# Kernel optimization log

Measured on AMD Instinct MI355X. Metric: run time of the kernel, lower is better.

Reference implementation:

```python
import jax, jax.numpy as jnp
import numpy as np


def setup_inputs() -> dict:
    key = jax.random.key(0)
    k1, k2 = jax.random.split(key)
    B, N, M = 16, 4096, 4096
    xyz1 = jax.random.normal(k1, (B, N, 3), dtype=jnp.float32)
    xyz2 = jax.random.normal(k2, (B, M, 3), dtype=jnp.float32)
    return {"xyz1": xyz1, "xyz2": xyz2}


def reference(xyz1, xyz2):
    sq1 = jnp.sum(xyz1 * xyz1, axis=-1)            # [B, N]
    sq2 = jnp.sum(xyz2 * xyz2, axis=-1)            # [B, M]
    inner = jnp.einsum('bnd,bmd->bnm', xyz1, xyz2)  # [B, N, M]
    d = sq1[:, :, None] + sq2[:, None, :] - 2.0 * inner
    dist1 = jnp.min(d, axis=2)  # nearest in xyz2 for each point of xyz1, [B, N]
    dist2 = jnp.min(d, axis=1)  # nearest in xyz1 for each point of xyz2, [B, M]
    return (jnp.mean(dist1), jnp.mean(dist2))
```

## Files before the change

kernel.cpp:

```cpp
#include <hip/hip_runtime.h>
#include <float.h>

#define BATCH  16
#define NPTS   4096
#define TOTALP (BATCH * NPTS)
#define NQ     (2 * TOTALP)

typedef _Float16 half8  __attribute__((ext_vector_type(8)));
typedef float    f32x16 __attribute__((ext_vector_type(16)));

#define ONE2 0x3C003C00u

__device__ __forceinline__ unsigned enc(float f)
{
    unsigned b = __float_as_uint(f);
    return (b & 0x80000000u) ? ~b : (b | 0x80000000u);
}
__device__ __forceinline__ float dec(unsigned k)
{
    return (k & 0x80000000u) ? __uint_as_float(k & 0x7FFFFFFFu)
                             : __uint_as_float(~k);
}

__device__ __forceinline__ unsigned pk(_Float16 lo, _Float16 hi)
{
    const unsigned a = (unsigned)__builtin_bit_cast(unsigned short, lo);
    const unsigned b = (unsigned)__builtin_bit_cast(unsigned short, hi);
    return a | (b << 16);
}

__device__ __forceinline__ float min16(const f32x16& d, float acc)
{
    const float m1 = fminf(fminf(d[0],  d[1]),  d[2]);
    const float m2 = fminf(fminf(d[3],  d[4]),  d[5]);
    const float m3 = fminf(fminf(d[6],  d[7]),  d[8]);
    const float m4 = fminf(fminf(d[9],  d[10]), d[11]);
    const float m5 = fminf(fminf(d[12], d[13]), d[14]);
    const float m6 = fminf(fminf(m1, m2), m3);
    const float m7 = fminf(fminf(m4, m5), d[15]);
    return fminf(fminf(m6, m7), acc);
}

__global__ __launch_bounds__(256) void prep_kernel(
    const float* __restrict__ xyz1, const float* __restrict__ xyz2,
    uint4* __restrict__ packQ, uint4* __restrict__ planes,
    unsigned* __restrict__ keys, float* __restrict__ out)
{
    const int i = blockIdx.x * 256 + threadIdx.x;
    if (i == 0) { out[0] = 0.0f; out[1] = 0.0f; }
    keys[i] = 0xFFFFFFFFu;

    const float* src = (i < TOTALP) ? xyz1 : xyz2;
    const int p = i & (TOTALP - 1);
    const float x = src[3 * p + 0];
    const float y = src[3 * p + 1];
    const float z = src[3 * p + 2];
    const float sq = x * x + y * y + z * z;
    const _Float16 sh = (_Float16)sq;
    const _Float16 sl = (_Float16)(sq - (float)sh);

    const _Float16 vxh = (_Float16)x, vyh = (_Float16)y, vzh = (_Float16)z;
    const _Float16 vxl = (_Float16)(x - (float)vxh);
    const _Float16 vyl = (_Float16)(y - (float)vyh);
    const _Float16 vzl = (_Float16)(z - (float)vzh);
    planes[i]      = make_uint4(pk(vxh, vyh), pk(vzh, vxh),
                                pk(vyh, vzh), pk(vxl, vyl));
    planes[NQ + i] = make_uint4(pk(vzl, vxl), pk(vyl, vzl),
                                ONE2,         pk(sh, sl));

    const float ux = -2.0f * x, uy = -2.0f * y, uz = -2.0f * z;
    const _Float16 uxh = (_Float16)ux, uyh = (_Float16)uy, uzh = (_Float16)uz;
    const _Float16 uxl = (_Float16)(ux - (float)uxh);
    const _Float16 uyl = (_Float16)(uy - (float)uyh);
    const _Float16 uzl = (_Float16)(uz - (float)uzh);
    packQ[i] = make_uint4(pk(uxh, uyh), pk(uzh, uxl), pk(uyl, uzl), pk(sh, sl));
}

__global__ __launch_bounds__(256, 4) void chamfer_stream(
    const uint4* __restrict__ packQ, const uint4* __restrict__ planes,
    unsigned* __restrict__ keys)
{
    const int blk = blockIdx.x;
    const int ch  = blk & 7;
    const int qc  = (blk >> 3) & 7;
    const int b   = (blk >> 6) & 15;
    const int dir = blk >> 10;

    const int lane = threadIdx.x & 63;
    const int wv   = threadIdx.x >> 6;
    const int n32  = lane & 31;
    const int half = lane >> 5;

    const int qbase = dir * TOTALP + b * NPTS + qc * 512 + wv * 128;
    half8 bfrag[4];
#pragma unroll
    for (int qf = 0; qf < 4; ++qf) {
        const uint4 d = packQ[qbase + qf * 32 + n32];
        const uint4 u = half ? make_uint4(d.y, d.z, d.w, ONE2)
                             : make_uint4(d.x, d.y, d.z, d.x);
        bfrag[qf] = __builtin_bit_cast(half8, u);
    }

    float acc[4];
#pragma unroll
    for (int qf = 0; qf < 4; ++qf) acc[qf] = FLT_MAX;

    f32x16 cz;
#pragma unroll
    for (int r = 0; r < 16; ++r) cz[r] = 0.0f;

    const uint4* __restrict__ ap =
        planes + (size_t)half * NQ + (dir ^ 1) * TOTALP + b * NPTS + ch * 512;

    uint4 t0 = ap[0 * 32 + n32];
    uint4 t1 = ap[1 * 32 + n32];
    uint4 t2 = ap[2 * 32 + n32];
    uint4 t3 = ap[3 * 32 + n32];

    for (int t = 0; t < 16; ++t) {
        const uint4 tn = ap[(((t + 4) & 15) * 32) + n32];
        const half8 af = __builtin_bit_cast(half8, t0);
#pragma unroll
        for (int qf = 0; qf < 4; ++qf) {
            const f32x16 dd = __builtin_amdgcn_mfma_f32_32x32x16_f16(
                af, bfrag[qf], cz, 0, 0, 0);
            acc[qf] = min16(dd, acc[qf]);
        }
        t0 = t1; t1 = t2; t2 = t3; t3 = tn;
    }

#pragma unroll
    for (int qf = 0; qf < 4; ++qf) {
        float v = acc[qf];
        v = fminf(v, __shfl_xor(v, 32));
        if (lane < 32)
            atomicMin(&keys[qbase + qf * 32 + n32], enc(v));
    }
}

__global__ __launch_bounds__(256) void chamfer_final_atomic(
    const unsigned* __restrict__ keys, float* __restrict__ out)
{
    const int q0  = blockIdx.x * 512 + threadIdx.x;
    const int dir = q0 >> 16;

    float d = dec(keys[q0]) + dec(keys[q0 + 256]);

    for (int off = 32; off > 0; off >>= 1)
        d += __shfl_down(d, off);

    __shared__ float wsum[4];
    const int lane = threadIdx.x & 63;
    const int wv   = threadIdx.x >> 6;
    if (lane == 0) wsum[wv] = d;
    __syncthreads();
    if (threadIdx.x == 0) {
        float s = wsum[0] + wsum[1] + wsum[2] + wsum[3];
        atomicAdd(&out[dir], s * (1.0f / (float)TOTALP));
    }
}

__global__ void zero_out_kernel(float* __restrict__ out)
{
    if (threadIdx.x == 0) { out[0] = 0.0f; out[1] = 0.0f; }
}

__global__ __launch_bounds__(256) void chamfer_raw_kernel(
    const float* __restrict__ xyz1, const float* __restrict__ xyz2,
    float* __restrict__ out)
{
    const int blk = blockIdx.x;
    const int dir = blk >> 8;
    const int idx = blk & 255;
    const int b   = idx >> 4;
    const int n0  = (idx & 15) << 8;

    const float* __restrict__ own = (dir == 0 ? xyz1 : xyz2) + (size_t)b * NPTS * 3;
    const float* __restrict__ opp = (dir == 0 ? xyz2 : xyz1) + (size_t)b * NPTS * 3;

    const int n = n0 + threadIdx.x;
    const float ax = own[3 * n + 0];
    const float ay = own[3 * n + 1];
    const float az = own[3 * n + 2];

    float best = FLT_MAX;
    for (int m = 0; m < NPTS; m += 4) {
#pragma unroll
        for (int u = 0; u < 4; ++u) {
            const float px = opp[3 * (m + u) + 0];
            const float py = opp[3 * (m + u) + 1];
            const float pz = opp[3 * (m + u) + 2];
            const float dx = px - ax, dy = py - ay, dz = pz - az;
            float d = dx * dx;
            d = fmaf(dy, dy, d);
            d = fmaf(dz, dz, d);
            best = fminf(best, d);
        }
    }

    float d = best;
    for (int off = 32; off > 0; off >>= 1)
        d += __shfl_down(d, off);

    __shared__ float wsum[4];
    const int lane = threadIdx.x & 63;
    const int wv   = threadIdx.x >> 6;
    if (lane == 0) wsum[wv] = d;
    __syncthreads();
    if (threadIdx.x == 0) {
        float s = wsum[0] + wsum[1] + wsum[2] + wsum[3];
        atomicAdd(&out[dir], s * (1.0f / (float)TOTALP));
    }
}

extern "C" void kernel_launch(void* const* d_in, const int* in_sizes, int n_in,
                              void* d_out, int out_size, void* d_ws, size_t ws_size,
                              hipStream_t stream)
{
    const float* xyz1 = (const float*)d_in[0];
    const float* xyz2 = (const float*)d_in[1];
    float* out = (float*)d_out;

    const size_t keys_bytes  = (size_t)NQ * sizeof(unsigned);
    const size_t packQ_bytes = (size_t)NQ * sizeof(uint4);
    const size_t plane_bytes = (size_t)2 * NQ * sizeof(uint4);

    if (ws_size >= keys_bytes + packQ_bytes + plane_bytes) {
        unsigned* keys   = (unsigned*)d_ws;
        uint4*    packQ  = (uint4*)((char*)d_ws + keys_bytes);
        uint4*    planes = (uint4*)((char*)d_ws + keys_bytes + packQ_bytes);

        prep_kernel<<<NQ / 256, 256, 0, stream>>>(xyz1, xyz2, packQ, planes, keys, out);
        chamfer_stream<<<2048, 256, 0, stream>>>(packQ, planes, keys);
        chamfer_final_atomic<<<NQ / 512, 256, 0, stream>>>(keys, out);
    } else {
        zero_out_kernel<<<1, 64, 0, stream>>>(out);
        chamfer_raw_kernel<<<512, 256, 0, stream>>>(xyz1, xyz2, out);
    }
}
```

Baseline: 84.63 us.

## Fuse min and mean reduction by giving each wave the full opponent set

Each wave now scans all 4096 opponent points for its 32 queries instead of one 512-point chunk. The per-query minimum is therefore complete inside the kernel and can be summed into the output directly. This removes the keys buffer, its initialisation, the atomicMin encoding and the separate final reduction kernel, and the sum is halved to correct for both lane halves contributing. In exchange, the grid is half as large and each loaded opponent tile feeds one MFMA instead of four, which raises load traffic per MFMA and lowers occupancy.

```diff
diff --git a/kernel.cpp b/kernel.cpp
--- a/kernel.cpp
+++ b/kernel.cpp
@@ -10,17 +10,6 @@
 typedef float    f32x16 __attribute__((ext_vector_type(16)));
 
 #define ONE2 0x3C003C00u
-
-__device__ __forceinline__ unsigned enc(float f)
-{
-    unsigned b = __float_as_uint(f);
-    return (b & 0x80000000u) ? ~b : (b | 0x80000000u);
-}
-__device__ __forceinline__ float dec(unsigned k)
-{
-    return (k & 0x80000000u) ? __uint_as_float(k & 0x7FFFFFFFu)
-                             : __uint_as_float(~k);
-}
 
 __device__ __forceinline__ unsigned pk(_Float16 lo, _Float16 hi)
 {
@@ -44,11 +33,10 @@
 __global__ __launch_bounds__(256) void prep_kernel(
     const float* __restrict__ xyz1, const float* __restrict__ xyz2,
     uint4* __restrict__ packQ, uint4* __restrict__ planes,
-    unsigned* __restrict__ keys, float* __restrict__ out)
+    float* __restrict__ out)
 {
     const int i = blockIdx.x * 256 + threadIdx.x;
     if (i == 0) { out[0] = 0.0f; out[1] = 0.0f; }
-    keys[i] = 0xFFFFFFFFu;
 
     const float* src = (i < TOTALP) ? xyz1 : xyz2;
     const int p = i & (TOTALP - 1);
@@ -76,87 +64,61 @@
     packQ[i] = make_uint4(pk(uxh, uyh), pk(uzh, uxl), pk(uyl, uzl), pk(sh, sl));
 }
 
-__global__ __launch_bounds__(256, 4) void chamfer_stream(
+__global__ __launch_bounds__(256, 4) void chamfer_fused(
     const uint4* __restrict__ packQ, const uint4* __restrict__ planes,
-    unsigned* __restrict__ keys)
+    float* __restrict__ out)
 {
+    __shared__ float wsum[4];
+
     const int blk = blockIdx.x;
-    const int ch  = blk & 7;
-    const int qc  = (blk >> 3) & 7;
-    const int b   = (blk >> 6) & 15;
-    const int dir = blk >> 10;
+    const int qc  = blk & 31;
+    const int b   = (blk >> 5) & 15;
+    const int dir = blk >> 9;
 
     const int lane = threadIdx.x & 63;
     const int wv   = threadIdx.x >> 6;
     const int n32  = lane & 31;
     const int half = lane >> 5;
 
-    const int qbase = dir * TOTALP + b * NPTS + qc * 512 + wv * 128;
-    half8 bfrag[4];
-#pragma unroll
-    for (int qf = 0; qf < 4; ++qf) {
-        const uint4 d = packQ[qbase + qf * 32 + n32];
-        const uint4 u = half ? make_uint4(d.y, d.z, d.w, ONE2)
-                             : make_uint4(d.x, d.y, d.z, d.x);
-        bfrag[qf] = __builtin_bit_cast(half8, u);
-    }
+    const int qbase = dir * TOTALP + b * NPTS + qc * 128 + wv * 32;
+    const uint4 d = packQ[qbase + n32];
+    const uint4 u = half ? make_uint4(d.y, d.z, d.w, ONE2)
+                         : make_uint4(d.x, d.y, d.z, d.x);
+    const half8 bfrag = __builtin_bit_cast(half8, u);
 
-    float acc[4];
-#pragma unroll
-    for (int qf = 0; qf < 4; ++qf) acc[qf] = FLT_MAX;
+    float acc = FLT_MAX;
 
     f32x16 cz;
 #pragma unroll
     for (int r = 0; r < 16; ++r) cz[r] = 0.0f;
 
     const uint4* __restrict__ ap =
-        planes + (size_t)half * NQ + (dir ^ 1) * TOTALP + b * NPTS + ch * 512;
+        planes + (size_t)half * NQ + (dir ^ 1) * TOTALP + b * NPTS;
 
     uint4 t0 = ap[0 * 32 + n32];
     uint4 t1 = ap[1 * 32 + n32];
     uint4 t2 = ap[2 * 32 + n32];
     uint4 t3 = ap[3 * 32 + n32];
 
-    for (int t = 0; t < 16; ++t) {
-        const uint4 tn = ap[(((t + 4) & 15) * 32) + n32];
+#pragma unroll 4
+    for (int t = 0; t < 128; ++t) {
+        const uint4 tn = ap[(((t + 4) & 127) * 32) + n32];
         const half8 af = __builtin_bit_cast(half8, t0);
-#pragma unroll
-        for (int qf = 0; qf < 4; ++qf) {
-            const f32x16 dd = __builtin_amdgcn_mfma_f32_32x32x16_f16(
-                af, bfrag[qf], cz, 0, 0, 0);
-            acc[qf] = min16(dd, acc[qf]);
-        }
+        const f32x16 dd = __builtin_amdgcn_mfma_f32_32x32x16_f16(
+            af, bfrag, cz, 0, 0, 0);
+        acc = min16(dd, acc);
         t0 = t1; t1 = t2; t2 = t3; t3 = tn;
     }
 
-#pragma unroll
-    for (int qf = 0; qf < 4; ++qf) {
-        float v = acc[qf];
-        v = fminf(v, __shfl_xor(v, 32));
-        if (lane < 32)
-            atomicMin(&keys[qbase + qf * 32 + n32], enc(v));
-    }
-}
+    float v = fminf(acc, __shfl_xor(acc, 32));
+    for (int off = 32; off > 0; off >>= 1)
+        v += __shfl_down(v, off);
 
-__global__ __launch_bounds__(256) void chamfer_final_atomic(
-    const unsigned* __restrict__ keys, float* __restrict__ out)
-{
-    const int q0  = blockIdx.x * 512 + threadIdx.x;
-    const int dir = q0 >> 16;
-
-    float d = dec(keys[q0]) + dec(keys[q0 + 256]);
-
-    for (int off = 32; off > 0; off >>= 1)
-        d += __shfl_down(d, off);
-
-    __shared__ float wsum[4];
-    const int lane = threadIdx.x & 63;
-    const int wv   = threadIdx.x >> 6;
-    if (lane == 0) wsum[wv] = d;
+    if (lane == 0) wsum[wv] = v;
     __syncthreads();
     if (threadIdx.x == 0) {
-        float s = wsum[0] + wsum[1] + wsum[2] + wsum[3];
-        atomicAdd(&out[dir], s * (1.0f / (float)TOTALP));
+        const float s = wsum[0] + wsum[1] + wsum[2] + wsum[3];
+        atomicAdd(&out[dir], s * (0.5f / (float)TOTALP));
     }
 }
 
@@ -221,18 +183,15 @@
     const float* xyz2 = (const float*)d_in[1];
     float* out = (float*)d_out;
 
-    const size_t keys_bytes  = (size_t)NQ * sizeof(unsigned);
     const size_t packQ_bytes = (size_t)NQ * sizeof(uint4);
     const size_t plane_bytes = (size_t)2 * NQ * sizeof(uint4);
 
-    if (ws_size >= keys_bytes + packQ_bytes + plane_bytes) {
-        unsigned* keys   = (unsigned*)d_ws;
-        uint4*    packQ  = (uint4*)((char*)d_ws + keys_bytes);
-        uint4*    planes = (uint4*)((char*)d_ws + keys_bytes + packQ_bytes);
+    if (ws_size >= packQ_bytes + plane_bytes) {
+        uint4* packQ  = (uint4*)d_ws;
+        uint4* planes = (uint4*)((char*)d_ws + packQ_bytes);
 
-        prep_kernel<<<NQ / 256, 256, 0, stream>>>(xyz1, xyz2, packQ, planes, keys, out);
-        chamfer_stream<<<2048, 256, 0, stream>>>(packQ, planes, keys);
-        chamfer_final_atomic<<<NQ / 512, 256, 0, stream>>>(keys, out);
+        prep_kernel<<<NQ / 256, 256, 0, stream>>>(xyz1, xyz2, packQ, planes, out);
+        chamfer_fused<<<1024, 256, 0, stream>>>(packQ, planes, out);
     } else {
         zero_out_kernel<<<1, 64, 0, stream>>>(out);
         chamfer_raw_kernel<<<512, 256, 0, stream>>>(xyz1, xyz2, out);
```

Measured after the change: 91.60 us. 1.08x slower.
